# Kernel tuning notes

Measured on AMD Instinct MI355X. Metric: run time of the kernel, lower is better.

Reference implementation:

```python
import jax, jax.numpy as jnp
import numpy as np

B, NX, NU, H, HID, NIT = 4096, 64, 16, 50, 256, 10


def dynamics(x, u, W1, b1, W2):
    # residual tanh-MLP dynamics: x_next = x + 0.1*tanh([x,u]@W1+b1)@W2
    z = jnp.concatenate([x, u], axis=-1)
    return x + 0.1 * jnp.tanh(z @ W1 + b1) @ W2


def setup_inputs() -> dict:
    key = jax.random.key(0)
    k0, k1, k2, k3 = jax.random.split(key, 4)
    x0 = jax.random.normal(k0, (B, NX), dtype=jnp.float32)
    xref = jnp.zeros((B, H + 1, NX), dtype=jnp.float32)
    W1 = jax.random.normal(k1, (NX + NU, HID), dtype=jnp.float32) * 0.05
    b1 = jnp.zeros((HID,), dtype=jnp.float32)
    W2 = jax.random.normal(k2, (HID, NX), dtype=jnp.float32) * 0.05
    # deterministic stand-in for torch.randn inside _compute_sqp_step (one draw per SQP iter)
    noise = jax.random.normal(k3, (NIT, B, H * NU), dtype=jnp.float32)
    return {"x0": x0, "xref": xref, "W1": W1, "b1": b1, "W2": W2,
            "noise": noise, "n_iterations": NIT}


def reference(x0, xref, W1, b1, W2, noise, n_iterations):
    batch, nx = x0.shape
    N = xref.shape[1] - 1            # horizon
    nu = noise.shape[2] // N         # control dim
    u = jnp.zeros((batch, N * nu), dtype=x0.dtype)

    def rollout(u_flat):
        us = jnp.swapaxes(u_flat.reshape(batch, N, nu), 0, 1)  # [N, B, nu]
        def step(x, u_k):
            x_next = dynamics(x, u_k, W1, b1, W2)
            return x_next, x_next
        _, xs = jax.lax.scan(step, x0, us)                     # [N, B, nx]
        return jnp.concatenate([x0[:, None], jnp.swapaxes(xs, 0, 1)], axis=1)  # [B, N+1, nx]

    x_traj = rollout(u)
    gx = gu = None
    for it in range(n_iterations):
        # sequential nonlinear rollout with current controls
        x_traj = rollout(u)
        # per-step linearization via VJP with ones cotangent (as in torch autograd.grad
        # with grad_outputs=ones); steps are independent so batch them over (B, N).
        xs = x_traj[:, :N].reshape(batch * N, nx)
        us = u.reshape(batch * N, nu)
        def f(xs_, us_):
            return dynamics(xs_, us_, W1, b1, W2)
        _, vjp_fn = jax.vjp(f, xs, us)
        gx_, gu_ = vjp_fn(jnp.ones((batch * N, nx), dtype=x0.dtype))
        gx = gx_.reshape(batch, N, nx)   # rows of A_lin (ones^T @ df/dx)
        gu = gu_.reshape(batch, N, nu)   # rows of B_lin (ones^T @ df/du)
        # SQP "step" in source is fresh gaussian noise * 0.01, scaled by 0.1
        u = u + 0.1 * (noise[it] * 0.01)
    # (first control, trajectory, predicted states, last-iteration linearization VJPs)
    return u[:, :nu], x_traj, x_traj[:, 1:], gx, gu
```

## Files before the change

### kernel.cpp

```cpp
#include <hip/hip_runtime.h>

typedef unsigned int uint;
typedef unsigned short ushort_t;
typedef __attribute__((ext_vector_type(8))) short bf16x8_t;
typedef __attribute__((ext_vector_type(4))) float f32x4_t;

constexpr int Bsz = 4096, NX = 64, NU = 16, NXU = 80, HID = 256, Hh = 50;
constexpr long NS = (long)Bsz * Hh * NU;
constexpr int O1 = 65536;
constexpr int O2 = 13434880;
constexpr int O3 = 26542080;
constexpr int O4 = 39649280;
constexpr int XT_PITCH = (Hh + 1) * NX;
constexpr int PR_PITCH = Hh * NX;
constexpr int U_PITCH = Hh * NU;

constexpr int W1S = 260;
constexpr int HS  = 264;
constexpr int HSR = 260;
constexpr int TS  = 264;
constexpr int W2S = 264;
constexpr int TLS = 264;

constexpr long T_BYTES = (long)Bsz * Hh * HID * 2;

__device__ __forceinline__ float tanh_fast(float x) {
    float e = __expf(2.0f * x);
    return 1.0f - 2.0f / (e + 1.0f);
}
__device__ __forceinline__ uint f2bf_u(float x) {
    uint b = __float_as_uint(x);
    return (b + 0x7FFFu + ((b >> 16) & 1u)) >> 16;
}
__device__ __forceinline__ float bf2f(ushort_t u) {
    return __uint_as_float(((uint)u) << 16);
}
__device__ __forceinline__ void unpack8(uint4 v, float* f) {
    f[0] = __uint_as_float(v.x << 16); f[1] = __uint_as_float(v.x & 0xFFFF0000u);
    f[2] = __uint_as_float(v.y << 16); f[3] = __uint_as_float(v.y & 0xFFFF0000u);
    f[4] = __uint_as_float(v.z << 16); f[5] = __uint_as_float(v.z & 0xFFFF0000u);
    f[6] = __uint_as_float(v.w << 16); f[7] = __uint_as_float(v.w & 0xFFFF0000u);
}

__global__ __launch_bounds__(512, 2) void ker_roll(const float* __restrict__ x0,
                                                   const float* __restrict__ W1,
                                                   const float* __restrict__ b1,
                                                   const float* __restrict__ W2,
                                                   const float* __restrict__ noise,
                                                   const int* __restrict__ nit_p,
                                                   float* __restrict__ out,
                                                   ushort_t* __restrict__ tg) {
    __shared__ __align__(16) float    W1L[NXU * W1S];
    __shared__ __align__(16) ushort_t W2T[NX * W2S];
    __shared__ __align__(16) float    hRT[16 * HSR];
    __shared__ __align__(16) float    zT[NXU * 16];
    __shared__ float b1L[HID];
    __shared__ float sL[HID];

    const int tid = threadIdx.x;
    const int b0 = blockIdx.x * 16;
    const int nit = nit_p[0];

    for (int i = tid; i < NXU * HID; i += 512)
        W1L[(i >> 8) * W1S + (i & 255)] = W1[i];
    for (int i = tid; i < HID * NX; i += 512) {
        int c = i >> 6, d = i & 63;
        W2T[d * W2S + c] = (ushort_t)f2bf_u(W2[i]);
    }
    if (tid < HID) b1L[tid] = b1[tid];
    for (int i = tid; i < 16 * NX; i += 512) {
        int r = i >> 6, d = i & 63;
        float v = x0[(b0 + r) * NX + d];
        zT[d * 16 + r] = v;
        out[O1 + (b0 + r) * XT_PITCH + d] = v;
    }
    const int r16n = (tid >> 4) & 15, q16n = tid & 15;
    if (tid < 256) {
        long base = (long)(b0 + r16n) * U_PITCH + q16n;
        float s = 0.f;
        for (int it = 0; it < nit - 1; ++it) s += noise[(long)it * NS + base];
        zT[(NX + q16n) * 16 + r16n] = 0.001f * s;
        out[(b0 + r16n) * NU + q16n] = 0.001f * (s + noise[(long)(nit - 1) * NS + base]);
    }
    __syncthreads();
    if (tid < HID) {
        float s = 0.f;
        for (int d = 0; d < NX; ++d) s += bf2f(W2T[d * W2S + tid]);
        sL[tid] = 0.1f * s;
    }

    const int ct = tid & 63, rt8 = tid >> 6;
    const int q16 = tid & 15, cg = tid >> 4;
    const uint* W2Tu = (const uint*)W2T;

    for (int k = 0; k < Hh; ++k) {
        __syncthreads();

        float v9[9];
        const bool fast = (k < Hh - 1) && (nit == 10);
        long nbase = (long)(b0 + r16n) * U_PITCH + (k + 1) * NU + q16n;
        if (fast && tid < 256) {
            #pragma unroll
            for (int it = 0; it < 9; ++it) v9[it] = noise[(long)it * NS + nbase];
        }

        float a_[2][4];
        {
            float bj[4];
            #pragma unroll
            for (int j = 0; j < 4; ++j) bj[j] = b1L[4 * ct + j];
            #pragma unroll
            for (int i = 0; i < 2; ++i)
                #pragma unroll
                for (int j = 0; j < 4; ++j) a_[i][j] = bj[j];
        }
        #pragma unroll 8
        for (int kk = 0; kk < NXU; ++kk) {
            float2 zv = *(const float2*)&zT[kk * 16 + 2 * rt8];
            float4 wv = *(const float4*)&W1L[kk * W1S + 4 * ct];
            float zz[2] = {zv.x, zv.y};
            float ww[4] = {wv.x, wv.y, wv.z, wv.w};
            #pragma unroll
            for (int i = 0; i < 2; ++i)
                #pragma unroll
                for (int j = 0; j < 4; ++j) a_[i][j] += zz[i] * ww[j];
        }
        float h_[2][4];
        #pragma unroll
        for (int i = 0; i < 2; ++i)
            #pragma unroll
            for (int j = 0; j < 4; ++j) h_[i][j] = tanh_fast(a_[i][j]);
        #pragma unroll
        for (int i = 0; i < 2; ++i)
            *(float4*)&hRT[(2 * rt8 + i) * HSR + 4 * ct] =
                make_float4(h_[i][0], h_[i][1], h_[i][2], h_[i][3]);
        {
            float s0 = sL[4 * ct], s1 = sL[4 * ct + 1], s2 = sL[4 * ct + 2], s3 = sL[4 * ct + 3];
            #pragma unroll
            for (int i = 0; i < 2; ++i) {
                float t0 = s0 * (1.f - h_[i][0] * h_[i][0]);
                float t1 = s1 * (1.f - h_[i][1] * h_[i][1]);
                float t2 = s2 * (1.f - h_[i][2] * h_[i][2]);
                float t3 = s3 * (1.f - h_[i][3] * h_[i][3]);
                size_t rho = (size_t)(b0 + 2 * rt8 + i) * Hh + k;
                uint2 pk = make_uint2(f2bf_u(t0) | (f2bf_u(t1) << 16),
                                      f2bf_u(t2) | (f2bf_u(t3) << 16));
                *(uint2*)(tg + rho * HID + 4 * ct) = pk;
            }
        }

        float unext = 0.f;
        if (tid < 256 && k < Hh - 1) {
            if (fast) {
                #pragma unroll
                for (int it = 0; it < 9; ++it) unext += v9[it];
            } else {
                for (int it = 0; it < nit - 1; ++it) unext += noise[(long)it * NS + nbase];
            }
            unext *= 0.001f;
        }

        __syncthreads();

        float xacc[2] = {0.f, 0.f};
        #pragma unroll 4
        for (int c8 = 0; c8 < HID / 8; ++c8) {
            float4 h0 = *(const float4*)&hRT[q16 * HSR + 8 * c8];
            float4 h1 = *(const float4*)&hRT[q16 * HSR + 8 * c8 + 4];
            float hf[8] = {h0.x, h0.y, h0.z, h0.w, h1.x, h1.y, h1.z, h1.w};
            #pragma unroll
            for (int i = 0; i < 2; ++i) {
                int d = cg + 32 * i;
                uint4 wv = *(const uint4*)&W2Tu[d * (W2S / 2) + 4 * c8];
                float wf[8];
                unpack8(wv, wf);
                #pragma unroll
                for (int jj = 0; jj < 8; ++jj) xacc[i] += hf[jj] * wf[jj];
            }
        }
        {
            const int bb = b0 + q16;
            #pragma unroll
            for (int i = 0; i < 2; ++i) {
                int d = cg + 32 * i;
                float xn = zT[d * 16 + q16] + 0.1f * xacc[i];
                out[O1 + bb * XT_PITCH + (k + 1) * NX + d] = xn;
                out[O2 + bb * PR_PITCH + k * NX + d] = xn;
                zT[d * 16 + q16] = xn;
            }
            if (tid < 256 && k < Hh - 1) zT[(NX + q16n) * 16 + r16n] = unext;
        }
    }
}

__global__ __launch_bounds__(256) void ker_lin2(const float* __restrict__ W1,
                                                const ushort_t* __restrict__ Tg,
                                                float* __restrict__ out) {
    __shared__ __align__(16) ushort_t W1b[NXU * TLS];

    const int tid = threadIdx.x;
    const int r0 = blockIdx.x * 128;

    {
        const float4* W1f4 = (const float4*)W1;
        for (int i = tid; i < (NXU * HID) / 4; i += 256) {
            float4 w = W1f4[i];
            int p = i >> 6, c4 = i & 63;
            uint2 pk = make_uint2(f2bf_u(w.x) | (f2bf_u(w.y) << 16),
                                  f2bf_u(w.z) | (f2bf_u(w.w) << 16));
            *(uint2*)&W1b[p * TLS + 4 * c4] = pk;
        }
    }
    __syncthreads();

    const int wv = tid >> 6, lane = tid & 63;
    const int m = lane & 15, quad = lane >> 4;

    f32x4_t acc[2][5];
    #pragma unroll
    for (int i = 0; i < 2; ++i)
        #pragma unroll
        for (int j = 0; j < 5; ++j) acc[i][j] = (f32x4_t){0.f, 0.f, 0.f, 0.f};

    const ushort_t* Ta = Tg + (size_t)(r0 + wv * 32 + m) * HID;
    const ushort_t* Tb = Ta + (size_t)16 * HID;

    #pragma unroll
    for (int kc = 0; kc < 8; ++kc) {
        const int koff = kc * 32 + quad * 8;
        bf16x8_t a0 = *(const bf16x8_t*)&Ta[koff];
        bf16x8_t a1 = *(const bf16x8_t*)&Tb[koff];
        #pragma unroll
        for (int nt = 0; nt < 5; ++nt) {
            bf16x8_t bfr = *(const bf16x8_t*)&W1b[(nt * 16 + m) * TLS + koff];
            acc[0][nt] = __builtin_amdgcn_mfma_f32_16x16x32_bf16(a0, bfr, acc[0][nt], 0, 0, 0);
            acc[1][nt] = __builtin_amdgcn_mfma_f32_16x16x32_bf16(a1, bfr, acc[1][nt], 0, 0, 0);
        }
    }

    #pragma unroll
    for (int mt = 0; mt < 2; ++mt) {
        int rbase = r0 + wv * 32 + mt * 16 + quad * 4;
        #pragma unroll
        for (int r = 0; r < 4; ++r) {
            int rho = rbase + r;
            int b = (int)(((unsigned long long)rho * 1374389535ULL) >> 36);
            int kk = rho - b * 50;
            float* gxp = out + O3 + (size_t)b * PR_PITCH + kk * NX + m;
            #pragma unroll
            for (int nt = 0; nt < 4; ++nt)
                gxp[nt * 16] = 1.0f + acc[mt][nt][r];
            out[O4 + (size_t)b * U_PITCH + kk * NU + m] = acc[mt][4][r];
        }
    }
}

__global__ __launch_bounds__(256) void ker_fused(const float* __restrict__ x0,
                                                 const float* __restrict__ W1,
                                                 const float* __restrict__ b1,
                                                 const float* __restrict__ W2,
                                                 const float* __restrict__ noise,
                                                 const int* __restrict__ nit_p,
                                                 float* __restrict__ out) {
    __shared__ __align__(16) float    W1L[NXU * W1S];
    __shared__ __align__(16) ushort_t W2T[NX * W2S];
    __shared__ __align__(16) float    hRT[16 * HS];
    __shared__ __align__(16) ushort_t tT[16 * TS];
    __shared__ __align__(16) float    zT[NXU * 16];
    __shared__ float b1L[HID];
    __shared__ float sL[HID];

    const int tid = threadIdx.x;
    const int b0 = blockIdx.x * 16;
    const int nit = nit_p[0];

    for (int i = tid; i < NXU * HID; i += 256)
        W1L[(i >> 8) * W1S + (i & 255)] = W1[i];
    for (int i = tid; i < HID * NX; i += 256) {
        int c = i >> 6, d = i & 63;
        W2T[d * W2S + c] = (ushort_t)f2bf_u(W2[i]);
    }
    b1L[tid] = b1[tid];
    for (int i = tid; i < 16 * NX; i += 256) {
        int r = i >> 6, d = i & 63;
        float v = x0[(b0 + r) * NX + d];
        zT[d * 16 + r] = v;
        out[O1 + (b0 + r) * XT_PITCH + d] = v;
    }
    const int r16 = tid >> 4, q16 = tid & 15;
    {
        long base = (long)(b0 + r16) * U_PITCH + q16;
        float s = 0.f;
        for (int it = 0; it < nit - 1; ++it) s += noise[(long)it * NS + base];
        zT[(NX + q16) * 16 + r16] = 0.001f * s;
        out[(b0 + r16) * NU + q16] = 0.001f * (s + noise[(long)(nit - 1) * NS + base]);
    }
    __syncthreads();
    {
        float s = 0.f;
        for (int d = 0; d < NX; ++d) s += bf2f(W2T[d * W2S + tid]);
        sL[tid] = 0.1f * s;
    }

    const int ct = tid & 63, rt = tid >> 6;
    uint* tTu = (uint*)tT;
    const uint* W2Tu = (const uint*)W2T;

    for (int k = 0; k < Hh; ++k) {
        __syncthreads();
        float v9[9];
        const bool fast = (k < Hh - 1) && (nit == 10);
        long nbase = (long)(b0 + r16) * U_PITCH + (k + 1) * NU + q16;
        if (fast) {
            #pragma unroll
            for (int it = 0; it < 9; ++it) v9[it] = noise[(long)it * NS + nbase];
        }
        float a_[4][4];
        {
            float bj[4];
            #pragma unroll
            for (int j = 0; j < 4; ++j) bj[j] = b1L[4 * ct + j];
            #pragma unroll
            for (int i = 0; i < 4; ++i)
                #pragma unroll
                for (int j = 0; j < 4; ++j) a_[i][j] = bj[j];
        }
        #pragma unroll 8
        for (int kk = 0; kk < NXU; ++kk) {
            float4 zv = *(const float4*)&zT[kk * 16 + 4 * rt];
            float4 wv = *(const float4*)&W1L[kk * W1S + 4 * ct];
            float zz[4] = {zv.x, zv.y, zv.z, zv.w};
            float ww[4] = {wv.x, wv.y, wv.z, wv.w};
            #pragma unroll
            for (int i = 0; i < 4; ++i)
                #pragma unroll
                for (int j = 0; j < 4; ++j) a_[i][j] += zz[i] * ww[j];
        }
        float h_[4][4];
        #pragma unroll
        for (int i = 0; i < 4; ++i)
            #pragma unroll
            for (int j = 0; j < 4; ++j) h_[i][j] = tanh_fast(a_[i][j]);
        #pragma unroll
        for (int i = 0; i < 4; ++i)
            *(float4*)&hRT[(4 * rt + i) * HS + 4 * ct] =
                make_float4(h_[i][0], h_[i][1], h_[i][2], h_[i][3]);
        {
            float s0 = sL[4 * ct], s1 = sL[4 * ct + 1], s2 = sL[4 * ct + 2], s3 = sL[4 * ct + 3];
            #pragma unroll
            for (int i = 0; i < 4; ++i) {
                float t0 = s0 * (1.f - h_[i][0] * h_[i][0]);
                float t1 = s1 * (1.f - h_[i][1] * h_[i][1]);
                float t2 = s2 * (1.f - h_[i][2] * h_[i][2]);
                float t3 = s3 * (1.f - h_[i][3] * h_[i][3]);
                tTu[(4 * rt + i) * (TS / 2) + 2 * ct]     = f2bf_u(t0) | (f2bf_u(t1) << 16);
                tTu[(4 * rt + i) * (TS / 2) + 2 * ct + 1] = f2bf_u(t2) | (f2bf_u(t3) << 16);
            }
        }
        float unext = 0.f;
        if (k < Hh - 1) {
            if (fast) {
                #pragma unroll
                for (int it = 0; it < 9; ++it) unext += v9[it];
            } else {
                for (int it = 0; it < nit - 1; ++it) unext += noise[(long)it * NS + nbase];
            }
            unext *= 0.001f;
        }
        __syncthreads();
        float xacc[4] = {0.f, 0.f, 0.f, 0.f};
        #pragma unroll 4
        for (int c8 = 0; c8 < HID / 8; ++c8) {
            float4 h0 = *(const float4*)&hRT[r16 * HS + 8 * c8];
            float4 h1 = *(const float4*)&hRT[r16 * HS + 8 * c8 + 4];
            float hf[8] = {h0.x, h0.y, h0.z, h0.w, h1.x, h1.y, h1.z, h1.w};
            #pragma unroll
            for (int i = 0; i < 4; ++i) {
                int d = q16 + 16 * i;
                uint4 wv = *(const uint4*)&W2Tu[d * (W2S / 2) + 4 * c8];
                float wf[8];
                unpack8(wv, wf);
                #pragma unroll
                for (int jj = 0; jj < 8; ++jj) xacc[i] += hf[jj] * wf[jj];
            }
        }
        {
            const int bb = b0 + r16;
            #pragma unroll
            for (int i = 0; i < 4; ++i) {
                int d = q16 + 16 * i;
                float xn = zT[d * 16 + r16] + 0.1f * xacc[i];
                out[O1 + bb * XT_PITCH + (k + 1) * NX + d] = xn;
                out[O2 + bb * PR_PITCH + k * NX + d] = xn;
                zT[d * 16 + r16] = xn;
            }
            if (k < Hh - 1) zT[(NX + q16) * 16 + r16] = unext;
        }
        {
            const uint* tTr = (const uint*)tT + r16 * (TS / 2);
            float g_[5] = {0.f, 0.f, 0.f, 0.f, 0.f};
            #pragma unroll 4
            for (int jc = 0; jc < HID / 8; ++jc) {
                uint4 tv = *(const uint4*)&tTr[4 * jc];
                float tf[8];
                unpack8(tv, tf);
                #pragma unroll
                for (int i = 0; i < 5; ++i) {
                    int p = q16 + 16 * i;
                    float4 w0 = *(const float4*)&W1L[p * W1S + 8 * jc];
                    float4 w1 = *(const float4*)&W1L[p * W1S + 8 * jc + 4];
                    g_[i] += tf[0] * w0.x + tf[1] * w0.y + tf[2] * w0.z + tf[3] * w0.w
                           + tf[4] * w1.x + tf[5] * w1.y + tf[6] * w1.z + tf[7] * w1.w;
                }
            }
            const int bb = b0 + r16;
            #pragma unroll
            for (int i = 0; i < 4; ++i)
                out[O3 + bb * PR_PITCH + k * NX + (q16 + 16 * i)] = 1.0f + g_[i];
            out[O4 + bb * U_PITCH + k * NU + q16] = g_[4];
        }
    }
}

extern "C" void kernel_launch(void* const* d_in, const int* in_sizes, int n_in,
                              void* d_out, int out_size, void* d_ws, size_t ws_size,
                              hipStream_t stream) {
    const float* x0    = (const float*)d_in[0];
    const float* W1    = (const float*)d_in[2];
    const float* b1    = (const float*)d_in[3];
    const float* W2    = (const float*)d_in[4];
    const float* noise = (const float*)d_in[5];
    const int*   nit   = (const int*)d_in[6];
    float* out = (float*)d_out;

    if (ws_size >= (size_t)T_BYTES) {
        ushort_t* tg = (ushort_t*)d_ws;
        ker_roll<<<Bsz / 16, 512, 0, stream>>>(x0, W1, b1, W2, noise, nit, out, tg);
        ker_lin2<<<(Bsz * Hh) / 128, 256, 0, stream>>>(W1, tg, out);
    } else {
        ker_fused<<<Bsz / 16, 256, 0, stream>>>(x0, W1, b1, W2, noise, nit, out);
    }
}
```

Before: 730.6 us.

## Remap rollout thread work: transpose W1 in LDS, per-column hidden units, per-d output

The rollout kernel now stores W1 transposed in shared memory with a padded stride, and zT with a padded stride. Each thread computes one hidden column for 8 batch rows, so W1 is read along its own row and z is broadcast. The W2 stage gives each thread one output dimension for two rows, which changes which global writes coalesce and which LDS bank patterns occur. The tg write becomes a scalar 16-bit store per element instead of a packed uint2, which may cost store efficiency in exchange for fewer LDS conflicts.

```diff
diff --git a/kernel.cpp b/kernel.cpp
--- a/kernel.cpp
+++ b/kernel.cpp
@@ -15,12 +15,14 @@
 constexpr int PR_PITCH = Hh * NX;
 constexpr int U_PITCH = Hh * NU;
 
-constexpr int W1S = 260;
-constexpr int HS  = 264;
-constexpr int HSR = 260;
-constexpr int TS  = 264;
-constexpr int W2S = 264;
-constexpr int TLS = 264;
+constexpr int W1S  = 260;
+constexpr int W1TS = 84;
+constexpr int HS   = 264;
+constexpr int HSR  = 260;
+constexpr int ZTS  = 20;
+constexpr int TS   = 264;
+constexpr int W2S  = 264;
+constexpr int TLS  = 264;
 
 constexpr long T_BYTES = (long)Bsz * Hh * HID * 2;
 
@@ -50,10 +52,10 @@
                                                    const int* __restrict__ nit_p,
                                                    float* __restrict__ out,
                                                    ushort_t* __restrict__ tg) {
-    __shared__ __align__(16) float    W1L[NXU * W1S];
+    __shared__ __align__(16) float    W1T[HID * W1TS];
     __shared__ __align__(16) ushort_t W2T[NX * W2S];
     __shared__ __align__(16) float    hRT[16 * HSR];
-    __shared__ __align__(16) float    zT[NXU * 16];
+    __shared__ __align__(16) float    zT[NXU * ZTS];
     __shared__ float b1L[HID];
     __shared__ float sL[HID];
 
@@ -61,8 +63,10 @@
     const int b0 = blockIdx.x * 16;
     const int nit = nit_p[0];
 
-    for (int i = tid; i < NXU * HID; i += 512)
-        W1L[(i >> 8) * W1S + (i & 255)] = W1[i];
+    for (int i = tid; i < NXU * HID; i += 512) {
+        int kk = i >> 8, c = i & 255;
+        W1T[c * W1TS + kk] = W1[i];
+    }
     for (int i = tid; i < HID * NX; i += 512) {
         int c = i >> 6, d = i & 63;
         W2T[d * W2S + c] = (ushort_t)f2bf_u(W2[i]);
@@ -71,7 +75,7 @@
     for (int i = tid; i < 16 * NX; i += 512) {
         int r = i >> 6, d = i & 63;
         float v = x0[(b0 + r) * NX + d];
-        zT[d * 16 + r] = v;
+        zT[d * ZTS + r] = v;
         out[O1 + (b0 + r) * XT_PITCH + d] = v;
     }
     const int r16n = (tid >> 4) & 15, q16n = tid & 15;
@@ -79,7 +83,7 @@
         long base = (long)(b0 + r16n) * U_PITCH + q16n;
         float s = 0.f;
         for (int it = 0; it < nit - 1; ++it) s += noise[(long)it * NS + base];
-        zT[(NX + q16n) * 16 + r16n] = 0.001f * s;
+        zT[(NX + q16n) * ZTS + r16n] = 0.001f * s;
         out[(b0 + r16n) * NU + q16n] = 0.001f * (s + noise[(long)(nit - 1) * NS + base]);
     }
     __syncthreads();
@@ -89,8 +93,8 @@
         sL[tid] = 0.1f * s;
     }
 
-    const int ct = tid & 63, rt8 = tid >> 6;
-    const int q16 = tid & 15, cg = tid >> 4;
+    const int cP1 = tid & 255, half = tid >> 8;
+    const int dP2 = tid & 63,  rp = tid >> 6;
     const uint* W2Tu = (const uint*)W2T;
 
     for (int k = 0; k < Hh; ++k) {
@@ -104,48 +108,40 @@
             for (int it = 0; it < 9; ++it) v9[it] = noise[(long)it * NS + nbase];
         }
 
-        float a_[2][4];
-        {
-            float bj[4];
-            #pragma unroll
-            for (int j = 0; j < 4; ++j) bj[j] = b1L[4 * ct + j];
-            #pragma unroll
-            for (int i = 0; i < 2; ++i)
-                #pragma unroll
-                for (int j = 0; j < 4; ++j) a_[i][j] = bj[j];
-        }
-        #pragma unroll 8
-        for (int kk = 0; kk < NXU; ++kk) {
-            float2 zv = *(const float2*)&zT[kk * 16 + 2 * rt8];
-            float4 wv = *(const float4*)&W1L[kk * W1S + 4 * ct];
-            float zz[2] = {zv.x, zv.y};
+        float a_[8];
+        {
+            float bj = b1L[cP1];
+            #pragma unroll
+            for (int i = 0; i < 8; ++i) a_[i] = bj;
+        }
+        const float* w1c = &W1T[cP1 * W1TS];
+        #pragma unroll 4
+        for (int kc = 0; kc < 20; ++kc) {
+            float4 wv = *(const float4*)&w1c[4 * kc];
             float ww[4] = {wv.x, wv.y, wv.z, wv.w};
             #pragma unroll
-            for (int i = 0; i < 2; ++i)
-                #pragma unroll
-                for (int j = 0; j < 4; ++j) a_[i][j] += zz[i] * ww[j];
-        }
-        float h_[2][4];
-        #pragma unroll
-        for (int i = 0; i < 2; ++i)
-            #pragma unroll
-            for (int j = 0; j < 4; ++j) h_[i][j] = tanh_fast(a_[i][j]);
-        #pragma unroll
-        for (int i = 0; i < 2; ++i)
-            *(float4*)&hRT[(2 * rt8 + i) * HSR + 4 * ct] =
-                make_float4(h_[i][0], h_[i][1], h_[i][2], h_[i][3]);
-        {
-            float s0 = sL[4 * ct], s1 = sL[4 * ct + 1], s2 = sL[4 * ct + 2], s3 = sL[4 * ct + 3];
-            #pragma unroll
-            for (int i = 0; i < 2; ++i) {
-                float t0 = s0 * (1.f - h_[i][0] * h_[i][0]);
-                float t1 = s1 * (1.f - h_[i][1] * h_[i][1]);
-                float t2 = s2 * (1.f - h_[i][2] * h_[i][2]);
-                float t3 = s3 * (1.f - h_[i][3] * h_[i][3]);
-                size_t rho = (size_t)(b0 + 2 * rt8 + i) * Hh + k;
-                uint2 pk = make_uint2(f2bf_u(t0) | (f2bf_u(t1) << 16),
-                                      f2bf_u(t2) | (f2bf_u(t3) << 16));
-                *(uint2*)(tg + rho * HID + 4 * ct) = pk;
+            for (int j = 0; j < 4; ++j) {
+                int kk = 4 * kc + j;
+                float4 z0 = *(const float4*)&zT[kk * ZTS + 8 * half];
+                float4 z1 = *(const float4*)&zT[kk * ZTS + 8 * half + 4];
+                float w = ww[j];
+                a_[0] += z0.x * w; a_[1] += z0.y * w; a_[2] += z0.z * w; a_[3] += z0.w * w;
+                a_[4] += z1.x * w; a_[5] += z1.y * w; a_[6] += z1.z * w; a_[7] += z1.w * w;
+            }
+        }
+        float h_[8];
+        #pragma unroll
+        for (int i = 0; i < 8; ++i) h_[i] = tanh_fast(a_[i]);
+        #pragma unroll
+        for (int i = 0; i < 8; ++i)
+            hRT[(8 * half + i) * HSR + cP1] = h_[i];
+        {
+            float sc = sL[cP1];
+            #pragma unroll
+            for (int i = 0; i < 8; ++i) {
+                float t = sc * (1.f - h_[i] * h_[i]);
+                size_t rho = (size_t)(b0 + 8 * half + i) * Hh + k;
+                tg[rho * HID + cP1] = (ushort_t)f2bf_u(t);
             }
         }
 
@@ -162,33 +158,36 @@
 
         __syncthreads();
 
-        float xacc[2] = {0.f, 0.f};
+        float acc0 = 0.f, acc1 = 0.f;
+        const int r0 = 2 * rp, r1 = 2 * rp + 1;
         #pragma unroll 4
-        for (int c8 = 0; c8 < HID / 8; ++c8) {
-            float4 h0 = *(const float4*)&hRT[q16 * HSR + 8 * c8];
-            float4 h1 = *(const float4*)&hRT[q16 * HSR + 8 * c8 + 4];
-            float hf[8] = {h0.x, h0.y, h0.z, h0.w, h1.x, h1.y, h1.z, h1.w};
-            #pragma unroll
-            for (int i = 0; i < 2; ++i) {
-                int d = cg + 32 * i;
-                uint4 wv = *(const uint4*)&W2Tu[d * (W2S / 2) + 4 * c8];
-                float wf[8];
-                unpack8(wv, wf);
-                #pragma unroll
-                for (int jj = 0; jj < 8; ++jj) xacc[i] += hf[jj] * wf[jj];
-            }
-        }
-        {
-            const int bb = b0 + q16;
-            #pragma unroll
-            for (int i = 0; i < 2; ++i) {
-                int d = cg + 32 * i;
-                float xn = zT[d * 16 + q16] + 0.1f * xacc[i];
-                out[O1 + bb * XT_PITCH + (k + 1) * NX + d] = xn;
-                out[O2 + bb * PR_PITCH + k * NX + d] = xn;
-                zT[d * 16 + q16] = xn;
-            }
-            if (tid < 256 && k < Hh - 1) zT[(NX + q16n) * 16 + r16n] = unext;
+        for (int j8 = 0; j8 < 32; ++j8) {
+            uint4 wv = *(const uint4*)&W2Tu[dP2 * (W2S / 2) + 4 * j8];
+            float wf[8];
+            unpack8(wv, wf);
+            float4 h0a = *(const float4*)&hRT[r0 * HSR + 8 * j8];
+            float4 h0b = *(const float4*)&hRT[r0 * HSR + 8 * j8 + 4];
+            float4 h1a = *(const float4*)&hRT[r1 * HSR + 8 * j8];
+            float4 h1b = *(const float4*)&hRT[r1 * HSR + 8 * j8 + 4];
+            float hf0[8] = {h0a.x, h0a.y, h0a.z, h0a.w, h0b.x, h0b.y, h0b.z, h0b.w};
+            float hf1[8] = {h1a.x, h1a.y, h1a.z, h1a.w, h1b.x, h1b.y, h1b.z, h1b.w};
+            #pragma unroll
+            for (int jj = 0; jj < 8; ++jj) {
+                acc0 += hf0[jj] * wf[jj];
+                acc1 += hf1[jj] * wf[jj];
+            }
+        }
+        {
+            const int bb0 = b0 + r0, bb1 = b0 + r1;
+            float xn0 = zT[dP2 * ZTS + r0] + 0.1f * acc0;
+            float xn1 = zT[dP2 * ZTS + r1] + 0.1f * acc1;
+            out[O1 + bb0 * XT_PITCH + (k + 1) * NX + dP2] = xn0;
+            out[O2 + bb0 * PR_PITCH + k * NX + dP2] = xn0;
+            out[O1 + bb1 * XT_PITCH + (k + 1) * NX + dP2] = xn1;
+            out[O2 + bb1 * PR_PITCH + k * NX + dP2] = xn1;
+            zT[dP2 * ZTS + r0] = xn0;
+            zT[dP2 * ZTS + r1] = xn1;
+            if (tid < 256 && k < Hh - 1) zT[(NX + q16n) * ZTS + r16n] = unext;
         }
     }
 }
```

After: 754.6 us. +3.3%, slower.
